# Performance work log

Hardware: AMD Instinct MI355X
Metric: run time of the kernel (lower is better)

Reference implementation:

```python
import jax, jax.numpy as jnp
import numpy as np


def setup_inputs() -> dict:
    key = jax.random.key(0)
    ks = jax.random.split(key, 6)
    B, S, D, E, F = 4, 2048, 1024, 8, 2048
    return {
        "hidden_states": jax.random.normal(ks[0], (B, S, D), dtype=jnp.float32),
        "attention_mask": jnp.ones((B, S), dtype=jnp.int32),
        "router_w": jax.random.normal(ks[1], (D, E), dtype=jnp.float32) * (D ** -0.5),
        "w1": jax.random.normal(ks[2], (E, D, F), dtype=jnp.float32) * (D ** -0.5),
        "b1": jnp.zeros((E, F), dtype=jnp.float32),
        "w2": jax.random.normal(ks[3], (E, F, D), dtype=jnp.float32) * (F ** -0.5),
        "b2": jnp.zeros((E, D), dtype=jnp.float32),
        "top_k": 2,
    }


def reference(hidden_states, attention_mask, router_w, w1, b1, w2, b2, top_k):
    B, S, D = hidden_states.shape
    E = router_w.shape[1]
    # Router: logits -> softmax -> top-k -> renormalize weights (weights / weight_sum)
    logits = jnp.einsum('bsd,de->bse', hidden_states, router_w)          # [B,S,E]
    probs = jax.nn.softmax(logits, axis=-1)
    top_w, top_i = jax.lax.top_k(probs, top_k)                           # [B,S,k]
    top_w = top_w / jnp.sum(top_w, axis=-1, keepdims=True)
    # Dense combine weights: [B,S,E], zero except the selected experts
    combine = jnp.sum(jax.nn.one_hot(top_i, E, dtype=hidden_states.dtype)
                      * top_w[..., None], axis=-2)                       # [B,S,E]
    # All-expert MLP (ReLU), then weighted combine
    h = jax.nn.relu(jnp.einsum('bsd,edf->ebsf', hidden_states, w1)
                    + b1[:, None, None, :])                              # [E,B,S,F]
    y = jnp.einsum('ebsf,efd->ebsd', h, w2) + b2[:, None, None, :]       # [E,B,S,D]
    out = jnp.einsum('bse,ebsd->bsd', combine, y)                        # [B,S,D]
    # Masked tokens remain zero (as in the original Python loop)
    out = jnp.where((attention_mask != 0)[..., None], out, 0.0)
    return out
```

## Files before the change

kernel.cpp:

```cpp
#include <hip/hip_runtime.h>

typedef __attribute__((ext_vector_type(8))) short short8;
typedef __attribute__((ext_vector_type(4))) float floatx4;

static constexpr int D = 1024;
static constexpr int F = 2048;
static constexpr int E = 8;
static constexpr int TOK = 4 * 2048;
static constexpr int RTOT = 2 * TOK;
static constexpr int MT = 24;
static constexpr int RBLK = 512;

__device__ __forceinline__ unsigned short f2bf(float f) {
  unsigned int u = __float_as_uint(f);
  unsigned int r = (u + 0x7fffu + ((u >> 16) & 1u)) >> 16;
  return (unsigned short)r;
}

__device__ __forceinline__ void glds16(const unsigned short* g, unsigned short* l) {
  __builtin_amdgcn_global_load_lds(
      (const __attribute__((address_space(1))) void*)g,
      (__attribute__((address_space(3))) void*)l, 16, 0, 0);
}

__global__ __launch_bounds__(256) void router_kernel(
    const float* __restrict__ hs, const int* __restrict__ mask,
    const float* __restrict__ rw, int2* __restrict__ te, float2* __restrict__ tw,
    int* __restrict__ blkcnt, unsigned short* __restrict__ Xbf) {
  __shared__ float rwT[E][D];
  __shared__ int cnt[16];
  int tid = threadIdx.x;
  if (tid < 16) cnt[tid] = 0;
#pragma unroll
  for (int q = 0; q < 4; ++q) {
    int i = tid * 4 + q;
    float4 a = *(const float4*)(rw + (size_t)i * E);
    float4 b = *(const float4*)(rw + (size_t)i * E + 4);
    rwT[0][i] = a.x; rwT[1][i] = a.y; rwT[2][i] = a.z; rwT[3][i] = a.w;
    rwT[4][i] = b.x; rwT[5][i] = b.y; rwT[6][i] = b.z; rwT[7][i] = b.w;
  }
  __syncthreads();

  int lane = tid & 63, wid = tid >> 6;
  int tok0 = blockIdx.x * 16 + wid * 4;
#pragma unroll 1
  for (int tt = 0; tt < 4; ++tt) {
    int t = tok0 + tt;
    const float* x = hs + (size_t)t * D;
    float acc[E];
#pragma unroll
    for (int e = 0; e < E; ++e) acc[e] = 0.f;
#pragma unroll
    for (int j = 0; j < 4; ++j) {
      int i0 = j * 256 + lane * 4;
      float4 xv = *(const float4*)(x + i0);
      union { unsigned short u[4]; uint2 q; } p;
      p.u[0] = f2bf(xv.x); p.u[1] = f2bf(xv.y);
      p.u[2] = f2bf(xv.z); p.u[3] = f2bf(xv.w);
      *(uint2*)(Xbf + (size_t)t * D + i0) = p.q;
#pragma unroll
      for (int e = 0; e < E; ++e) {
        float4 rv = *(const float4*)&rwT[e][i0];
        acc[e] += xv.x * rv.x + xv.y * rv.y + xv.z * rv.z + xv.w * rv.w;
      }
    }
#pragma unroll
    for (int off = 32; off > 0; off >>= 1) {
#pragma unroll
      for (int e = 0; e < E; ++e) acc[e] += __shfl_xor(acc[e], off, 64);
    }
    if (lane == 0) {
      int i1 = 0;
#pragma unroll
      for (int e = 1; e < E; ++e) if (acc[e] > acc[i1]) i1 = e;
      int i2 = (i1 == 0) ? 1 : 0;
#pragma unroll
      for (int e = 0; e < E; ++e) if (e != i1 && acc[e] > acc[i2]) i2 = e;
      float mx = fmaxf(acc[i1], acc[i2]);
      float e1 = expf(acc[i1] - mx), e2 = expf(acc[i2] - mx);
      float s = e1 + e2;
      float m = (mask[t] != 0) ? 1.f : 0.f;
      te[t] = make_int2(i1, i2);
      tw[t] = make_float2(e1 / s * m, e2 / s * m);
      atomicAdd(&cnt[i1], 1);
      atomicAdd(&cnt[8 + i2], 1);
    }
  }
  __syncthreads();
  if (tid < 16) blkcnt[blockIdx.x * 16 + tid] = cnt[tid];
}

__global__ __launch_bounds__(256) void prefix_kernel(const int* __restrict__ blkcnt,
                                                     int* __restrict__ meta) {
  __shared__ int part[256];
  int tid = threadIdx.x;
  int c = tid & 15, g = tid >> 4;
  int s = 0;
  for (int b = g; b < RBLK; b += 16) s += blkcnt[b * 16 + c];
  part[tid] = s;
  __syncthreads();
  if (tid < 16) {
    int tot = 0;
#pragma unroll
    for (int g2 = 0; g2 < 16; ++g2) tot += part[g2 * 16 + tid];
    meta[tid] = tot;
  }
  __syncthreads();
  if (tid == 0) {
    int run = 0;
    for (int e = 0; e < E; ++e) {
      meta[16 + e] = run;
      meta[24 + e] = run + meta[e];
      run += meta[e] + meta[8 + e];
    }
  }
}

__global__ __launch_bounds__(256) void scatter_kernel(
    const int2* __restrict__ te, const float2* __restrict__ tw,
    int* __restrict__ meta, int* __restrict__ LIST, float* __restrict__ WTS) {
  int t = blockIdx.x * 256 + threadIdx.x;
  int lane = threadIdx.x & 63;
  int2 e = te[t];
  float2 w = tw[t];
#pragma unroll
  for (int ex = 0; ex < E; ++ex) {
    unsigned long long m1 = __ballot(e.x == ex);
    if (m1) {
      int leader = __ffsll((long long)m1) - 1;
      int base = 0;
      if (lane == leader) base = atomicAdd(&meta[32 + ex], (int)__popcll(m1));
      base = __shfl(base, leader, 64);
      if (e.x == ex) {
        int pos = (int)__popcll(m1 & ((1ull << lane) - 1ull));
        int s1 = meta[16 + ex] + base + pos;
        LIST[s1] = t; WTS[s1] = w.x;
      }
    }
    unsigned long long m2 = __ballot(e.y == ex);
    if (m2) {
      int leader = __ffsll((long long)m2) - 1;
      int base = 0;
      if (lane == leader) base = atomicAdd(&meta[40 + ex], (int)__popcll(m2));
      base = __shfl(base, leader, 64);
      if (e.y == ex) {
        int pos = (int)__popcll(m2 & ((1ull << lane) - 1ull));
        int s2 = meta[24 + ex] + base + pos;
        LIST[s2] = t; WTS[s2] = w.y;
      }
    }
  }
}

__global__ __launch_bounds__(256) void cvtw_kernel(const float* __restrict__ src,
                                                   unsigned short* __restrict__ dst,
                                                   int K, int N) {
  int e = blockIdx.x, k0 = blockIdx.y * 64, n0 = blockIdx.z * 64;
  src += (size_t)e * K * N;
  dst += (size_t)e * K * N;
  __shared__ float t[64][65];
  int tid = threadIdx.x;
  int tr = tid >> 4, tc = (tid & 15) * 4;
#pragma unroll
  for (int i = 0; i < 4; ++i) {
    int k = tr + i * 16;
    float4 v = *(const float4*)(src + (size_t)(k0 + k) * N + n0 + tc);
    t[k][tc] = v.x; t[k][tc + 1] = v.y; t[k][tc + 2] = v.z; t[k][tc + 3] = v.w;
  }
  __syncthreads();
  int n = tid >> 2, kk = (tid & 3) * 16;
  union { unsigned short u[16]; uint4 q[2]; } p;
#pragma unroll
  for (int j = 0; j < 16; ++j) p.u[j] = f2bf(t[kk + j][n]);
  uint4* o = (uint4*)(dst + (size_t)(n0 + n) * K + k0 + kk);
  o[0] = p.q[0]; o[1] = p.q[1];
}

__global__ __launch_bounds__(256) void gemm1_kernel(
    const unsigned short* __restrict__ X,
    const unsigned short* __restrict__ w1t,
    const float* __restrict__ b1,
    const int* __restrict__ LIST,
    const int* __restrict__ meta,
    unsigned short* __restrict__ Hc) {
  const int K = D, N = F;
  int bx = blockIdx.x;
  int e = bx & 7;
  int t = bx >> 3;
  int n0 = (t & 15) * 128;
  int m = t >> 4;
  int cnt = meta[e] + meta[8 + e];
  int mrow = m * 128;
  if (mrow >= cnt) return;
  int rowStart = meta[16 + e] + mrow;
  int rowsLeft = cnt - mrow; if (rowsLeft > 128) rowsLeft = 128;

  __shared__ unsigned short As[128 * 32];
  __shared__ unsigned short Bs[128 * 32];
  int tid = threadIdx.x;
  int lane = tid & 63, wid = tid >> 6;
  int wm = (wid >> 1) * 64, wn = (wid & 1) * 64;
  int lr = lane & 15, lq = lane >> 4;

  int r0 = wid * 16 + (lane >> 2), r1 = 64 + r0;
  int kc = (lane & 3) * 8;
  int c0 = r0 < rowsLeft ? r0 : rowsLeft - 1;
  int c1 = r1 < rowsLeft ? r1 : rowsLeft - 1;
  const unsigned short* gA0 = X + (size_t)LIST[rowStart + c0] * K + kc;
  const unsigned short* gA1 = X + (size_t)LIST[rowStart + c1] * K + kc;
  const unsigned short* wb = w1t + (size_t)e * N * K;
  const unsigned short* gB0 = wb + (size_t)(n0 + r0) * K + kc;
  const unsigned short* gB1 = wb + (size_t)(n0 + r1) * K + kc;
  unsigned short* lA0 = &As[r0 * 32 + kc];
  unsigned short* lA1 = &As[r1 * 32 + kc];
  unsigned short* lB0 = &Bs[r0 * 32 + kc];
  unsigned short* lB1 = &Bs[r1 * 32 + kc];

  floatx4 acc[4][4];
#pragma unroll
  for (int i = 0; i < 4; ++i)
#pragma unroll
    for (int j = 0; j < 4; ++j) acc[i][j] = (floatx4){0.f, 0.f, 0.f, 0.f};

  for (int k0 = 0; k0 < K; k0 += 32) {
    __syncthreads();
    glds16(gA0 + k0, lA0);
    glds16(gA1 + k0, lA1);
    glds16(gB0 + k0, lB0);
    glds16(gB1 + k0, lB1);
    __syncthreads();
    short8 af[4], bfr[4];
#pragma unroll
    for (int i = 0; i < 4; ++i)
      af[i] = *(const short8*)&As[(wm + i * 16 + lr) * 32 + lq * 8];
#pragma unroll
    for (int j = 0; j < 4; ++j)
      bfr[j] = *(const short8*)&Bs[(wn + j * 16 + lr) * 32 + lq * 8];
#pragma unroll
    for (int i = 0; i < 4; ++i)
#pragma unroll
      for (int j = 0; j < 4; ++j)
        acc[i][j] = __builtin_amdgcn_mfma_f32_16x16x32_bf16(af[i], bfr[j], acc[i][j], 0, 0, 0);
  }
  const float* be = b1 + (size_t)e * N;
#pragma unroll
  for (int i = 0; i < 4; ++i) {
#pragma unroll
    for (int j = 0; j < 4; ++j) {
      int col = n0 + wn + j * 16 + lr;
      float bias = be[col];
#pragma unroll
      for (int r = 0; r < 4; ++r) {
        int row = wm + i * 16 + lq * 4 + r;
        if (row < rowsLeft) {
          float v = fmaxf(acc[i][j][r] + bias, 0.f);
          Hc[(size_t)(rowStart + row) * N + col] = f2bf(v);
        }
      }
    }
  }
}

__global__ __launch_bounds__(256) void gemm2_kernel(
    const unsigned short* __restrict__ Hc,
    const unsigned short* __restrict__ w2t,
    const float* __restrict__ b2,
    const int* __restrict__ LIST, const float* __restrict__ WTS,
    const int* __restrict__ meta,
    float* __restrict__ out) {
  const int K = F, N = D;
  int bx = blockIdx.x;
  int e = bx & 7;
  int t = bx >> 3;
  int n0 = (t & 7) * 128;
  int m = t >> 3;
  int cnt = meta[e] + meta[8 + e];
  int mrow = m * 128;
  if (mrow >= cnt) return;
  int rowStart = meta[16 + e] + mrow;
  int rowsLeft = cnt - mrow; if (rowsLeft > 128) rowsLeft = 128;

  __shared__ unsigned short As[128 * 32];
  __shared__ unsigned short Bs[128 * 32];
  int tid = threadIdx.x;
  int lane = tid & 63, wid = tid >> 6;
  int wm = (wid >> 1) * 64, wn = (wid & 1) * 64;
  int lr = lane & 15, lq = lane >> 4;

  int r0 = wid * 16 + (lane >> 2), r1 = 64 + r0;
  int kc = (lane & 3) * 8;
  int c0 = r0 < rowsLeft ? r0 : rowsLeft - 1;
  int c1 = r1 < rowsLeft ? r1 : rowsLeft - 1;
  const unsigned short* gA0 = Hc + (size_t)(rowStart + c0) * K + kc;
  const unsigned short* gA1 = Hc + (size_t)(rowStart + c1) * K + kc;
  const unsigned short* wb = w2t + (size_t)e * N * K;
  const unsigned short* gB0 = wb + (size_t)(n0 + r0) * K + kc;
  const unsigned short* gB1 = wb + (size_t)(n0 + r1) * K + kc;
  unsigned short* lA0 = &As[r0 * 32 + kc];
  unsigned short* lA1 = &As[r1 * 32 + kc];
  unsigned short* lB0 = &Bs[r0 * 32 + kc];
  unsigned short* lB1 = &Bs[r1 * 32 + kc];

  floatx4 acc[4][4];
#pragma unroll
  for (int i = 0; i < 4; ++i)
#pragma unroll
    for (int j = 0; j < 4; ++j) acc[i][j] = (floatx4){0.f, 0.f, 0.f, 0.f};

  for (int k0 = 0; k0 < K; k0 += 32) {
    __syncthreads();
    glds16(gA0 + k0, lA0);
    glds16(gA1 + k0, lA1);
    glds16(gB0 + k0, lB0);
    glds16(gB1 + k0, lB1);
    __syncthreads();
    short8 af[4], bfr[4];
#pragma unroll
    for (int i = 0; i < 4; ++i)
      af[i] = *(const short8*)&As[(wm + i * 16 + lr) * 32 + lq * 8];
#pragma unroll
    for (int j = 0; j < 4; ++j)
      bfr[j] = *(const short8*)&Bs[(wn + j * 16 + lr) * 32 + lq * 8];
#pragma unroll
    for (int i = 0; i < 4; ++i)
#pragma unroll
      for (int j = 0; j < 4; ++j)
        acc[i][j] = __builtin_amdgcn_mfma_f32_16x16x32_bf16(af[i], bfr[j], acc[i][j], 0, 0, 0);
  }
  const float* be = b2 + (size_t)e * N;
#pragma unroll
  for (int i = 0; i < 4; ++i) {
    int tokr[4]; float wtr[4]; bool val[4];
#pragma unroll
    for (int r = 0; r < 4; ++r) {
      int row = wm + i * 16 + lq * 4 + r;
      val[r] = row < rowsLeft;
      int gi = rowStart + (val[r] ? row : 0);
      tokr[r] = LIST[gi]; wtr[r] = WTS[gi];
    }
#pragma unroll
    for (int j = 0; j < 4; ++j) {
      int col = n0 + wn + j * 16 + lr;
      float bias = be[col];
#pragma unroll
      for (int r = 0; r < 4; ++r) {
        if (val[r]) {
          atomicAdd(&out[(size_t)tokr[r] * N + col], wtr[r] * (acc[i][j][r] + bias));
        }
      }
    }
  }
}

extern "C" void kernel_launch(void* const* d_in, const int* in_sizes, int n_in,
                              void* d_out, int out_size, void* d_ws, size_t ws_size,
                              hipStream_t stream) {
  (void)in_sizes; (void)n_in; (void)ws_size;
  const float* hs   = (const float*)d_in[0];
  const int*   mask = (const int*)d_in[1];
  const float* rw   = (const float*)d_in[2];
  const float* w1   = (const float*)d_in[3];
  const float* b1   = (const float*)d_in[4];
  const float* w2   = (const float*)d_in[5];
  const float* b2   = (const float*)d_in[6];
  float* out = (float*)d_out;

  char* ws = (char*)d_ws;
  int* meta  = (int*)ws;
  int2* te   = (int2*)(ws + 1024);
  float2* tw = (float2*)(ws + 1024 + (size_t)TOK * 8);
  int* LIST  = (int*)(ws + 1024 + (size_t)TOK * 16);
  float* WTS = (float*)(ws + 1024 + (size_t)TOK * 16 + (size_t)RTOT * 4);
  int* blkcnt = (int*)(ws + (512 << 10));
  unsigned short* Xbf = (unsigned short*)(ws + (1 << 20));
  unsigned short* Hc  = (unsigned short*)(ws + (1 << 20) + (size_t)TOK * D * 2);
  unsigned short* Wt  = (unsigned short*)(ws + (1 << 20) + (size_t)TOK * D * 2 +
                                          (size_t)RTOT * F * 2);

  hipMemsetAsync(meta, 0, 256, stream);
  hipMemsetAsync(out, 0, (size_t)out_size * sizeof(float), stream);
  router_kernel<<<RBLK, 256, 0, stream>>>(hs, mask, rw, te, tw, blkcnt, Xbf);
  prefix_kernel<<<1, 256, 0, stream>>>(blkcnt, meta);
  scatter_kernel<<<TOK / 256, 256, 0, stream>>>(te, tw, meta, LIST, WTS);
  cvtw_kernel<<<dim3(E, D / 64, F / 64), 256, 0, stream>>>(w1, Wt, D, F);
  gemm1_kernel<<<E * MT * (F / 128), 256, 0, stream>>>(Xbf, Wt, b1, LIST, meta, Hc);
  cvtw_kernel<<<dim3(E, F / 64, D / 64), 256, 0, stream>>>(w2, Wt, F, D);
  gemm2_kernel<<<E * MT * (D / 128), 256, 0, stream>>>(Hc, Wt, b2, LIST, WTS, meta, out);
}
```

Baseline: 480.7 us.

## Replace gemm2 atomic scatter-add with per-slot stores and a combine kernel

Scatter now records, for each token, the slot index of each of its two expert rows. When the workspace is large enough, gemm2 writes weighted expert outputs into a dense per-slot fp32 buffer instead of doing atomicAdd into the output. A new combine kernel then sums each token's two slots into the output, which also removes the output memset. The aim is to avoid contended fp32 atomics, at the cost of an extra 64MB intermediate buffer written and read back; masked tokens would rely on their slot indices having been set.

```diff
diff --git a/kernel.cpp b/kernel.cpp
--- a/kernel.cpp
+++ b/kernel.cpp
@@ -118,7 +118,8 @@
 
 __global__ __launch_bounds__(256) void scatter_kernel(
     const int2* __restrict__ te, const float2* __restrict__ tw,
-    int* __restrict__ meta, int* __restrict__ LIST, float* __restrict__ WTS) {
+    int* __restrict__ meta, int* __restrict__ LIST, float* __restrict__ WTS,
+    int* __restrict__ slotp, int* __restrict__ slots) {
   int t = blockIdx.x * 256 + threadIdx.x;
   int lane = threadIdx.x & 63;
   int2 e = te[t];
@@ -134,7 +135,7 @@
       if (e.x == ex) {
         int pos = (int)__popcll(m1 & ((1ull << lane) - 1ull));
         int s1 = meta[16 + ex] + base + pos;
-        LIST[s1] = t; WTS[s1] = w.x;
+        LIST[s1] = t; WTS[s1] = w.x; slotp[t] = s1;
       }
     }
     unsigned long long m2 = __ballot(e.y == ex);
@@ -146,7 +147,7 @@
       if (e.y == ex) {
         int pos = (int)__popcll(m2 & ((1ull << lane) - 1ull));
         int s2 = meta[24 + ex] + base + pos;
-        LIST[s2] = t; WTS[s2] = w.y;
+        LIST[s2] = t; WTS[s2] = w.y; slots[t] = s2;
       }
     }
   }
@@ -261,13 +262,15 @@
   }
 }
 
+template <int MODE>
 __global__ __launch_bounds__(256) void gemm2_kernel(
     const unsigned short* __restrict__ Hc,
     const unsigned short* __restrict__ w2t,
     const float* __restrict__ b2,
     const int* __restrict__ LIST, const float* __restrict__ WTS,
     const int* __restrict__ meta,
-    float* __restrict__ out) {
+    float* __restrict__ out,
+    float* __restrict__ Yc) {
   const int K = F, N = D;
   int bx = blockIdx.x;
   int e = bx & 7;
@@ -336,7 +339,8 @@
       int row = wm + i * 16 + lq * 4 + r;
       val[r] = row < rowsLeft;
       int gi = rowStart + (val[r] ? row : 0);
-      tokr[r] = LIST[gi]; wtr[r] = WTS[gi];
+      if (MODE == 0) tokr[r] = LIST[gi];
+      wtr[r] = WTS[gi];
     }
 #pragma unroll
     for (int j = 0; j < 4; ++j) {
@@ -345,17 +349,36 @@
 #pragma unroll
       for (int r = 0; r < 4; ++r) {
         if (val[r]) {
-          atomicAdd(&out[(size_t)tokr[r] * N + col], wtr[r] * (acc[i][j][r] + bias));
+          float v = wtr[r] * (acc[i][j][r] + bias);
+          if (MODE == 0) {
+            atomicAdd(&out[(size_t)tokr[r] * N + col], v);
+          } else {
+            int row = wm + i * 16 + lq * 4 + r;
+            Yc[(size_t)(rowStart + row) * N + col] = v;
+          }
         }
       }
     }
   }
+}
+
+__global__ __launch_bounds__(256) void combine_kernel(
+    const float* __restrict__ Yc, const int* __restrict__ slotp,
+    const int* __restrict__ slots, float* __restrict__ out) {
+  int t = blockIdx.x;
+  int d4 = threadIdx.x * 4;
+  int s1 = slotp[t], s2 = slots[t];
+  float4 a = *(const float4*)(Yc + (size_t)s1 * D + d4);
+  float4 b = *(const float4*)(Yc + (size_t)s2 * D + d4);
+  float4 o;
+  o.x = a.x + b.x; o.y = a.y + b.y; o.z = a.z + b.z; o.w = a.w + b.w;
+  *(float4*)(out + (size_t)t * D + d4) = o;
 }
 
 extern "C" void kernel_launch(void* const* d_in, const int* in_sizes, int n_in,
                               void* d_out, int out_size, void* d_ws, size_t ws_size,
                               hipStream_t stream) {
-  (void)in_sizes; (void)n_in; (void)ws_size;
+  (void)in_sizes; (void)n_in;
   const float* hs   = (const float*)d_in[0];
   const int*   mask = (const int*)d_in[1];
   const float* rw   = (const float*)d_in[2];
@@ -371,19 +394,30 @@
   float2* tw = (float2*)(ws + 1024 + (size_t)TOK * 8);
   int* LIST  = (int*)(ws + 1024 + (size_t)TOK * 16);
   float* WTS = (float*)(ws + 1024 + (size_t)TOK * 16 + (size_t)RTOT * 4);
+  int* slotp = (int*)(ws + 1024 + (size_t)TOK * 16 + (size_t)RTOT * 8);
+  int* slots = (int*)(ws + 1024 + (size_t)TOK * 16 + (size_t)RTOT * 8 + (size_t)TOK * 4);
   int* blkcnt = (int*)(ws + (512 << 10));
   unsigned short* Xbf = (unsigned short*)(ws + (1 << 20));
   unsigned short* Hc  = (unsigned short*)(ws + (1 << 20) + (size_t)TOK * D * 2);
   unsigned short* Wt  = (unsigned short*)(ws + (1 << 20) + (size_t)TOK * D * 2 +
                                           (size_t)RTOT * F * 2);
+  size_t yc_off = (size_t)(1 << 20) + (size_t)TOK * D * 2 + (size_t)RTOT * F * 2 +
+                  (size_t)E * (size_t)D * F * 2;
+  float* Yc = (float*)(ws + yc_off);
+  bool wide = ws_size >= yc_off + (size_t)RTOT * D * 4;
 
   hipMemsetAsync(meta, 0, 256, stream);
-  hipMemsetAsync(out, 0, (size_t)out_size * sizeof(float), stream);
+  if (!wide) hipMemsetAsync(out, 0, (size_t)out_size * sizeof(float), stream);
   router_kernel<<<RBLK, 256, 0, stream>>>(hs, mask, rw, te, tw, blkcnt, Xbf);
   prefix_kernel<<<1, 256, 0, stream>>>(blkcnt, meta);
-  scatter_kernel<<<TOK / 256, 256, 0, stream>>>(te, tw, meta, LIST, WTS);
+  scatter_kernel<<<TOK / 256, 256, 0, stream>>>(te, tw, meta, LIST, WTS, slotp, slots);
   cvtw_kernel<<<dim3(E, D / 64, F / 64), 256, 0, stream>>>(w1, Wt, D, F);
   gemm1_kernel<<<E * MT * (F / 128), 256, 0, stream>>>(Xbf, Wt, b1, LIST, meta, Hc);
   cvtw_kernel<<<dim3(E, F / 64, D / 64), 256, 0, stream>>>(w2, Wt, F, D);
-  gemm2_kernel<<<E * MT * (D / 128), 256, 0, stream>>>(Hc, Wt, b2, LIST, WTS, meta, out);
-}
+  if (wide) {
+    gemm2_kernel<1><<<E * MT * (D / 128), 256, 0, stream>>>(Hc, Wt, b2, LIST, WTS, meta, out, Yc);
+    combine_kernel<<<TOK, 256, 0, stream>>>(Yc, slotp, slots, out);
+  } else {
+    gemm2_kernel<0><<<E * MT * (D / 128), 256, 0, stream>>>(Hc, Wt, b2, LIST, WTS, meta, out, Yc);
+  }
+}
```

Result: faster. 450.2 us (-6.3%).
